# Optimization experiments

Measured on AMD Instinct MI355X. Metric: run time of the kernel, lower is better.

Reference implementation:

```python
import jax, jax.numpy as jnp
import numpy as np

B, D_IN, N_CLASSES, N_NODES, D_2D = 512, 512, 16, 100000, 2
EPS = 1e-8  # torch cosine_similarity eps


def setup_inputs() -> dict:
    key = jax.random.key(0)
    k0, k1, k2, k3, k4 = jax.random.split(key, 5)
    logits = jax.random.normal(k0, (B, N_CLASSES), dtype=jnp.float32)
    train_data = jax.random.normal(k1, (B, D_IN), dtype=jnp.float32)
    all_nodes = jax.random.normal(k2, (N_NODES, N_CLASSES), dtype=jnp.float32)
    all_nodes_2d = jax.random.normal(k3, (N_NODES, D_2D), dtype=jnp.float32)
    W = jax.random.normal(k4, (D_IN, D_2D), dtype=jnp.float32) * 0.02
    b = jnp.zeros((D_2D,), dtype=jnp.float32)
    return {"logits": logits, "train_data": train_data, "all_nodes": all_nodes,
            "all_nodes_2d": all_nodes_2d, "W": W, "b": b}


def reference(logits, train_data, all_nodes, all_nodes_2d, W, b):
    # model(train_data): linear 512 -> 2 projection
    emb = train_data @ W + b                                  # (B, 2)
    probs = jax.nn.softmax(logits, axis=1)                    # (B, C)
    pred_class = jnp.argmax(probs, axis=1)                    # (B,)
    node_class = jnp.argmax(all_nodes, axis=1)                # (N,)

    # cosine similarity between each sample's probs and every node (B, N)
    p_norm = jnp.linalg.norm(probs, axis=1, keepdims=True)    # (B, 1)
    n_norm = jnp.linalg.norm(all_nodes, axis=1)               # (N,)
    sim = (probs @ all_nodes.T) / jnp.maximum(p_norm * n_norm[None, :], EPS)

    # masked nearest-neighbor search: only nodes whose argmax class matches
    # the sample's predicted class are candidates (equivalent to the per-sample
    # boolean filtering + argmax in the original loop; first-match tie-break).
    masked_sim = jnp.where(pred_class[:, None] == node_class[None, :], sim, -jnp.inf)
    closest = jnp.argmax(masked_sim, axis=1)                  # (B,)

    target = all_nodes_2d[closest]                            # (B, 2)
    per_sample_mse = jnp.mean((emb - target) ** 2, axis=1)    # (B,)
    return jnp.mean(per_sample_mse)                           # scalar
```

## Files before the change

### kernel.cpp

```cpp
#include <hip/hip_runtime.h>

#define BATCH 512
#define DIN 512
#define NCLS 16
#define NNODES 100000
#define CBLK 256
#define NODE_BLOCKS ((NNODES + CBLK - 1) / CBLK)

#define WS_VAL   0
#define WS_PROBS 1601536
#define WS_EMB   1634304
#define WS_PCLS  1638400
#define WS_MSE   1640448
#define WS_DONE  1642496

__device__ __forceinline__ unsigned ford(float f) {
    unsigned bits = __float_as_uint(f);
    return (bits & 0x80000000u) ? ~bits : (bits | 0x80000000u);
}

__global__ __launch_bounds__(512) void prep_kernel(
    const float* __restrict__ logits,
    const float* __restrict__ train_data,
    const float* __restrict__ W,
    const float* __restrict__ bvec,
    float* __restrict__ probs,
    float* __restrict__ emb,
    int* __restrict__ pcls,
    unsigned int* __restrict__ done) {
    if (blockIdx.x < 64) {
        const int wave = threadIdx.x >> 6;
        const int lane = threadIdx.x & 63;
        const int s = blockIdx.x * 8 + wave;
        const float* td = train_data + s * DIN;
        const float2* W2 = (const float2*)W;
        float a0 = 0.f, a1 = 0.f;
        for (int k = lane; k < DIN; k += 64) {
            float t = td[k];
            float2 w = W2[k];
            a0 += t * w.x;
            a1 += t * w.y;
        }
        for (int off = 32; off; off >>= 1) {
            a0 += __shfl_down(a0, off);
            a1 += __shfl_down(a1, off);
        }
        if (lane == 0) {
            emb[2 * s]     = a0 + bvec[0];
            emb[2 * s + 1] = a1 + bvec[1];
        }
    } else {
        const int s = threadIdx.x;
        const float4* lg = (const float4*)(logits + s * NCLS);
        float4 x0 = lg[0], x1 = lg[1], x2 = lg[2], x3 = lg[3];
        float v[NCLS] = {x0.x, x0.y, x0.z, x0.w, x1.x, x1.y, x1.z, x1.w,
                         x2.x, x2.y, x2.z, x2.w, x3.x, x3.y, x3.z, x3.w};
        float m = v[0];
        int pred = 0;
        #pragma unroll
        for (int j = 1; j < NCLS; ++j)
            if (v[j] > m) { m = v[j]; pred = j; }
        float sum = 0.f;
        #pragma unroll
        for (int j = 0; j < NCLS; ++j) { v[j] = expf(v[j] - m); sum += v[j]; }
        float inv = 1.0f / sum;
        float4* p4 = (float4*)(probs + s * NCLS);
        p4[0] = make_float4(v[0] * inv, v[1] * inv, v[2] * inv, v[3] * inv);
        p4[1] = make_float4(v[4] * inv, v[5] * inv, v[6] * inv, v[7] * inv);
        p4[2] = make_float4(v[8] * inv, v[9] * inv, v[10] * inv, v[11] * inv);
        p4[3] = make_float4(v[12] * inv, v[13] * inv, v[14] * inv, v[15] * inv);
        pcls[s] = pred;
        if (s == 0) *done = 0u;
    }
}

__global__ __launch_bounds__(256) void nodes_kernel(
    const float* __restrict__ all_nodes,
    const float* __restrict__ probs,
    const int* __restrict__ pcls,
    unsigned long long* __restrict__ val) {
    __shared__ float4 snode[4 * CBLK];
    __shared__ float sinv[CBLK];
    __shared__ unsigned short clist[NCLS * CBLK];
    __shared__ int scnt[NCLS];

    const int t = threadIdx.x;
    if (t < NCLS) scnt[t] = 0;
    __syncthreads();

    const int nid = blockIdx.x * CBLK + t;
    if (nid < NNODES) {
        const float4* nv = (const float4*)(all_nodes + nid * NCLS);
        float4 v0 = nv[0], v1 = nv[1], v2 = nv[2], v3 = nv[3];
        float vals[NCLS] = {v0.x, v0.y, v0.z, v0.w, v1.x, v1.y, v1.z, v1.w,
                            v2.x, v2.y, v2.z, v2.w, v3.x, v3.y, v3.z, v3.w};
        int cls = 0;
        float m = vals[0];
        float nrm2 = 0.f;
        #pragma unroll
        for (int j = 0; j < NCLS; ++j) {
            if (j > 0 && vals[j] > m) { m = vals[j]; cls = j; }
            nrm2 += vals[j] * vals[j];
        }
        snode[t]            = v0;
        snode[CBLK + t]     = v1;
        snode[2 * CBLK + t] = v2;
        snode[3 * CBLK + t] = v3;
        sinv[t] = 1.0f / sqrtf(nrm2);
        int pos = atomicAdd(&scnt[cls], 1);
        clist[cls * CBLK + pos] = (unsigned short)t;
    }
    __syncthreads();

    const int base = blockIdx.x * CBLK;
    #pragma unroll
    for (int h = 0; h < 2; ++h) {
        const int s = t + h * CBLK;
        const float4* p4 = (const float4*)(probs + s * NCLS);
        float4 a0 = p4[0], a1 = p4[1], a2 = p4[2], a3 = p4[3];
        const int c = pcls[s];
        const int cnt = scnt[c];
        const unsigned short* lst = &clist[c * CBLK];
        unsigned long long best = 0ull;
        for (int i = 0; i < cnt; ++i) {
            const int n = lst[i];
            float4 v0 = snode[n];
            float4 v1 = snode[CBLK + n];
            float4 v2 = snode[2 * CBLK + n];
            float4 v3 = snode[3 * CBLK + n];
            float dot = a0.x * v0.x + a0.y * v0.y + a0.z * v0.z + a0.w * v0.w
                      + a1.x * v1.x + a1.y * v1.y + a1.z * v1.z + a1.w * v1.w
                      + a2.x * v2.x + a2.y * v2.y + a2.z * v2.z + a2.w * v2.w
                      + a3.x * v3.x + a3.y * v3.y + a3.z * v3.z + a3.w * v3.w;
            float sim = dot * sinv[n];
            unsigned long long packed =
                ((unsigned long long)ford(sim) << 32)
                | (unsigned long long)(0xFFFFFFFFu - (unsigned)(base + n));
            best = (packed > best) ? packed : best;
        }
        val[blockIdx.x * BATCH + s] = best;
    }
}

__global__ __launch_bounds__(64) void merge_kernel(
    const unsigned long long* __restrict__ val,
    const float* __restrict__ emb,
    const float* __restrict__ all_nodes_2d,
    float* __restrict__ mse,
    unsigned int* __restrict__ done,
    float* __restrict__ out) {
    const int s = blockIdx.x;
    const int k = threadIdx.x;

    unsigned long long m = 0ull;
    for (int b = k; b < NODE_BLOCKS; b += 64) {
        unsigned long long v = val[b * BATCH + s];
        m = (v > m) ? v : m;
    }
    for (int off = 32; off; off >>= 1) {
        unsigned long long o = __shfl_down(m, off);
        m = (o > m) ? o : m;
    }
    if (k == 0) {
        int idx = (m == 0ull) ? 0
                              : (int)(0xFFFFFFFFu - (unsigned)(m & 0xFFFFFFFFull));
        float2 tg = ((const float2*)all_nodes_2d)[idx];
        float2 e = ((const float2*)emb)[s];
        float d0 = e.x - tg.x;
        float d1 = e.y - tg.y;
        mse[s] = 0.5f * (d0 * d0 + d1 * d1);
    }
    __threadfence();
    unsigned ticket = 0u;
    if (k == 0) ticket = atomicAdd(done, 1u);
    ticket = __shfl(ticket, 0);
    if (ticket == (unsigned)(gridDim.x - 1)) {
        __threadfence();
        float ssum = 0.f;
        for (int i = k; i < BATCH; i += 64) ssum += mse[i];
        for (int off = 32; off; off >>= 1) ssum += __shfl_down(ssum, off);
        if (k == 0) out[0] = ssum / (float)BATCH;
    }
}

extern "C" void kernel_launch(void* const* d_in, const int* in_sizes, int n_in,
                              void* d_out, int out_size, void* d_ws, size_t ws_size,
                              hipStream_t stream) {
    const float* logits       = (const float*)d_in[0];
    const float* train_data   = (const float*)d_in[1];
    const float* all_nodes    = (const float*)d_in[2];
    const float* all_nodes_2d = (const float*)d_in[3];
    const float* W            = (const float*)d_in[4];
    const float* bvec         = (const float*)d_in[5];
    float* out = (float*)d_out;

    char* ws = (char*)d_ws;
    unsigned long long* val = (unsigned long long*)(ws + WS_VAL);
    float* probs            = (float*)(ws + WS_PROBS);
    float* emb              = (float*)(ws + WS_EMB);
    int* pcls               = (int*)(ws + WS_PCLS);
    float* mse              = (float*)(ws + WS_MSE);
    unsigned int* done      = (unsigned int*)(ws + WS_DONE);

    prep_kernel<<<65, 512, 0, stream>>>(logits, train_data, W, bvec,
                                        probs, emb, pcls, done);

    nodes_kernel<<<NODE_BLOCKS, CBLK, 0, stream>>>(all_nodes, probs, pcls, val);

    merge_kernel<<<BATCH, 64, 0, stream>>>(val, emb, all_nodes_2d,
                                           mse, done, out);
}
```

Before: 107.9 us.

## Sort samples by predicted class to cut wave divergence; fuse embedding into merge

```diff
diff --git a/kernel.cpp b/kernel.cpp
--- a/kernel.cpp
+++ b/kernel.cpp
@@ -9,10 +9,10 @@
 
 #define WS_VAL   0
 #define WS_PROBS 1601536
-#define WS_EMB   1634304
-#define WS_PCLS  1638400
-#define WS_MSE   1640448
-#define WS_DONE  1642496
+#define WS_SORT  1634304
+#define WS_SCLS  1636352
+#define WS_MSE   1638400
+#define WS_DONE  1640448
 
 __device__ __forceinline__ unsigned ford(float f) {
     unsigned bits = __float_as_uint(f);
@@ -21,63 +21,54 @@
 
 __global__ __launch_bounds__(512) void prep_kernel(
     const float* __restrict__ logits,
-    const float* __restrict__ train_data,
-    const float* __restrict__ W,
-    const float* __restrict__ bvec,
     float* __restrict__ probs,
-    float* __restrict__ emb,
-    int* __restrict__ pcls,
+    int* __restrict__ sorted_ids,
+    int* __restrict__ slot_cls,
     unsigned int* __restrict__ done) {
-    if (blockIdx.x < 64) {
-        const int wave = threadIdx.x >> 6;
-        const int lane = threadIdx.x & 63;
-        const int s = blockIdx.x * 8 + wave;
-        const float* td = train_data + s * DIN;
-        const float2* W2 = (const float2*)W;
-        float a0 = 0.f, a1 = 0.f;
-        for (int k = lane; k < DIN; k += 64) {
-            float t = td[k];
-            float2 w = W2[k];
-            a0 += t * w.x;
-            a1 += t * w.y;
-        }
-        for (int off = 32; off; off >>= 1) {
-            a0 += __shfl_down(a0, off);
-            a1 += __shfl_down(a1, off);
-        }
-        if (lane == 0) {
-            emb[2 * s]     = a0 + bvec[0];
-            emb[2 * s + 1] = a1 + bvec[1];
-        }
-    } else {
-        const int s = threadIdx.x;
-        const float4* lg = (const float4*)(logits + s * NCLS);
-        float4 x0 = lg[0], x1 = lg[1], x2 = lg[2], x3 = lg[3];
-        float v[NCLS] = {x0.x, x0.y, x0.z, x0.w, x1.x, x1.y, x1.z, x1.w,
-                         x2.x, x2.y, x2.z, x2.w, x3.x, x3.y, x3.z, x3.w};
-        float m = v[0];
-        int pred = 0;
-        #pragma unroll
-        for (int j = 1; j < NCLS; ++j)
-            if (v[j] > m) { m = v[j]; pred = j; }
-        float sum = 0.f;
-        #pragma unroll
-        for (int j = 0; j < NCLS; ++j) { v[j] = expf(v[j] - m); sum += v[j]; }
-        float inv = 1.0f / sum;
-        float4* p4 = (float4*)(probs + s * NCLS);
-        p4[0] = make_float4(v[0] * inv, v[1] * inv, v[2] * inv, v[3] * inv);
-        p4[1] = make_float4(v[4] * inv, v[5] * inv, v[6] * inv, v[7] * inv);
-        p4[2] = make_float4(v[8] * inv, v[9] * inv, v[10] * inv, v[11] * inv);
-        p4[3] = make_float4(v[12] * inv, v[13] * inv, v[14] * inv, v[15] * inv);
-        pcls[s] = pred;
-        if (s == 0) *done = 0u;
-    }
+    __shared__ int scnt[NCLS];
+    __shared__ int soff[NCLS + 1];
+    const int s = threadIdx.x;
+    if (s < NCLS) scnt[s] = 0;
+    __syncthreads();
+
+    const float4* lg = (const float4*)(logits + s * NCLS);
+    float4 x0 = lg[0], x1 = lg[1], x2 = lg[2], x3 = lg[3];
+    float v[NCLS] = {x0.x, x0.y, x0.z, x0.w, x1.x, x1.y, x1.z, x1.w,
+                     x2.x, x2.y, x2.z, x2.w, x3.x, x3.y, x3.z, x3.w};
+    float m = v[0];
+    int pred = 0;
+    #pragma unroll
+    for (int j = 1; j < NCLS; ++j)
+        if (v[j] > m) { m = v[j]; pred = j; }
+    float sum = 0.f;
+    #pragma unroll
+    for (int j = 0; j < NCLS; ++j) { v[j] = expf(v[j] - m); sum += v[j]; }
+    float inv = 1.0f / sum;
+    float4* p4 = (float4*)(probs + s * NCLS);
+    p4[0] = make_float4(v[0] * inv, v[1] * inv, v[2] * inv, v[3] * inv);
+    p4[1] = make_float4(v[4] * inv, v[5] * inv, v[6] * inv, v[7] * inv);
+    p4[2] = make_float4(v[8] * inv, v[9] * inv, v[10] * inv, v[11] * inv);
+    p4[3] = make_float4(v[12] * inv, v[13] * inv, v[14] * inv, v[15] * inv);
+
+    int pos = atomicAdd(&scnt[pred], 1);
+    __syncthreads();
+    if (s == 0) {
+        int acc = 0;
+        for (int c = 0; c < NCLS; ++c) { soff[c] = acc; acc += scnt[c]; }
+        soff[NCLS] = acc;
+        *done = 0u;
+    }
+    __syncthreads();
+    const int slot = soff[pred] + pos;
+    sorted_ids[slot] = s;
+    slot_cls[slot] = pred;
 }
 
 __global__ __launch_bounds__(256) void nodes_kernel(
     const float* __restrict__ all_nodes,
     const float* __restrict__ probs,
-    const int* __restrict__ pcls,
+    const int* __restrict__ sorted_ids,
+    const int* __restrict__ slot_cls,
     unsigned long long* __restrict__ val) {
     __shared__ float4 snode[4 * CBLK];
     __shared__ float sinv[CBLK];
@@ -115,10 +106,11 @@
     const int base = blockIdx.x * CBLK;
     #pragma unroll
     for (int h = 0; h < 2; ++h) {
-        const int s = t + h * CBLK;
+        const int slot = t + h * CBLK;
+        const int s = sorted_ids[slot];
+        const int c = slot_cls[slot];
         const float4* p4 = (const float4*)(probs + s * NCLS);
         float4 a0 = p4[0], a1 = p4[1], a2 = p4[2], a3 = p4[3];
-        const int c = pcls[s];
         const int cnt = scnt[c];
         const unsigned short* lst = &clist[c * CBLK];
         unsigned long long best = 0ull;
@@ -138,36 +130,55 @@
                 | (unsigned long long)(0xFFFFFFFFu - (unsigned)(base + n));
             best = (packed > best) ? packed : best;
         }
-        val[blockIdx.x * BATCH + s] = best;
+        val[blockIdx.x * BATCH + slot] = best;
     }
 }
 
 __global__ __launch_bounds__(64) void merge_kernel(
+    const float* __restrict__ train_data,
+    const float* __restrict__ W,
+    const float* __restrict__ bvec,
+    const int* __restrict__ sorted_ids,
     const unsigned long long* __restrict__ val,
-    const float* __restrict__ emb,
     const float* __restrict__ all_nodes_2d,
     float* __restrict__ mse,
     unsigned int* __restrict__ done,
     float* __restrict__ out) {
-    const int s = blockIdx.x;
+    const int j = blockIdx.x;
     const int k = threadIdx.x;
+    const int s = sorted_ids[j];
+
+    float a0 = 0.f, a1 = 0.f;
+    const float* td = train_data + s * DIN;
+    const float2* W2 = (const float2*)W;
+    for (int kk = k; kk < DIN; kk += 64) {
+        float t = td[kk];
+        float2 w = W2[kk];
+        a0 += t * w.x;
+        a1 += t * w.y;
+    }
 
     unsigned long long m = 0ull;
     for (int b = k; b < NODE_BLOCKS; b += 64) {
-        unsigned long long v = val[b * BATCH + s];
+        unsigned long long v = val[b * BATCH + j];
         m = (v > m) ? v : m;
     }
+
     for (int off = 32; off; off >>= 1) {
+        a0 += __shfl_down(a0, off);
+        a1 += __shfl_down(a1, off);
         unsigned long long o = __shfl_down(m, off);
         m = (o > m) ? o : m;
     }
+
     if (k == 0) {
+        float e0 = a0 + bvec[0];
+        float e1 = a1 + bvec[1];
         int idx = (m == 0ull) ? 0
                               : (int)(0xFFFFFFFFu - (unsigned)(m & 0xFFFFFFFFull));
         float2 tg = ((const float2*)all_nodes_2d)[idx];
-        float2 e = ((const float2*)emb)[s];
-        float d0 = e.x - tg.x;
-        float d1 = e.y - tg.y;
+        float d0 = e0 - tg.x;
+        float d1 = e1 - tg.y;
         mse[s] = 0.5f * (d0 * d0 + d1 * d1);
     }
     __threadfence();
@@ -197,16 +208,17 @@
     char* ws = (char*)d_ws;
     unsigned long long* val = (unsigned long long*)(ws + WS_VAL);
     float* probs            = (float*)(ws + WS_PROBS);
-    float* emb              = (float*)(ws + WS_EMB);
-    int* pcls               = (int*)(ws + WS_PCLS);
+    int* sorted_ids         = (int*)(ws + WS_SORT);
+    int* slot_cls           = (int*)(ws + WS_SCLS);
     float* mse              = (float*)(ws + WS_MSE);
     unsigned int* done      = (unsigned int*)(ws + WS_DONE);
 
-    prep_kernel<<<65, 512, 0, stream>>>(logits, train_data, W, bvec,
-                                        probs, emb, pcls, done);
-
-    nodes_kernel<<<NODE_BLOCKS, CBLK, 0, stream>>>(all_nodes, probs, pcls, val);
-
-    merge_kernel<<<BATCH, 64, 0, stream>>>(val, emb, all_nodes_2d,
-                                           mse, done, out);
-}
+    prep_kernel<<<1, BATCH, 0, stream>>>(logits, probs, sorted_ids,
+                                         slot_cls, done);
+
+    nodes_kernel<<<NODE_BLOCKS, CBLK, 0, stream>>>(all_nodes, probs,
+                                                   sorted_ids, slot_cls, val);
+
+    merge_kernel<<<BATCH, 64, 0, stream>>>(train_data, W, bvec, sorted_ids,
+                                           val, all_nodes_2d, mse, done, out);
+}
```

Measured after the change: 106.7 us. About the same (-1.1%).
